# Kernel optimization log

Measured on AMD Instinct MI355X. Metric: run time of the kernel, lower is better.

Reference implementation:

```python
import jax, jax.numpy as jnp
import numpy as np

BIN_SIZE = 16
B, C, H, W = 32, 256, 64, 64


def _make_grid(lab):
    # Faithful vectorization of the per-batch loop in the torch module.
    # index = arange(bin) - bin//2
    idx = jnp.arange(BIN_SIZE, dtype=lab.dtype) - (BIN_SIZE // 2)
    # mesh_y[b, j] = 2*idx[j]*lab[b,0,3]/bin + (lab[b,0,1]*2 - 1)
    mesh_y = 2.0 * idx[None, :] * lab[:, 0, 3, None] / BIN_SIZE + (lab[:, 0, 1, None] * 2.0 - 1.0)
    # mesh_x[b, i] = 2*idx[i]*lab[b,0,4]/bin + (lab[b,0,2]*2 - 1)
    mesh_x = 2.0 * idx[None, :] * lab[:, 0, 4, None] / BIN_SIZE + (lab[:, 0, 2, None] * 2.0 - 1.0)
    b = lab.shape[0]
    # torch: grid_x, grid_y = meshgrid(mesh_x, mesh_y) with 'ij' indexing;
    # mesh_box[b,i,j,0] = grid_y[i,j] = mesh_y[j]; mesh_box[b,i,j,1] = grid_x[i,j] = mesh_x[i]
    g0 = jnp.broadcast_to(mesh_y[:, None, :], (b, BIN_SIZE, BIN_SIZE))  # x-coord channel
    g1 = jnp.broadcast_to(mesh_x[:, :, None], (b, BIN_SIZE, BIN_SIZE))  # y-coord channel
    return jnp.stack([g0, g1], axis=-1)  # [B, bin, bin, 2]


def _grid_sample(feat, grid):
    # Bilinear grid_sample, padding_mode='zeros', align_corners=False (torch defaults).
    Bb, Cc, Hh, Ww = feat.shape
    x = ((grid[..., 0] + 1.0) * Ww - 1.0) * 0.5  # [B, Hg, Wg]
    y = ((grid[..., 1] + 1.0) * Hh - 1.0) * 0.5
    x0f = jnp.floor(x)
    y0f = jnp.floor(y)
    x0 = x0f.astype(jnp.int32)
    y0 = y0f.astype(jnp.int32)
    x1 = x0 + 1
    y1 = y0 + 1
    wx1 = x - x0f
    wx0 = 1.0 - wx1
    wy1 = y - y0f
    wy0 = 1.0 - wy1
    bidx = jnp.arange(Bb)[:, None, None]

    def corner(xi, yi, wgt):
        valid = ((xi >= 0) & (xi < Ww) & (yi >= 0) & (yi < Hh)).astype(feat.dtype)
        xc = jnp.clip(xi, 0, Ww - 1)
        yc = jnp.clip(yi, 0, Hh - 1)
        v = feat[bidx, :, yc, xc]  # [B, Hg, Wg, C] (advanced indices pulled front)
        return v * (wgt * valid)[..., None]

    out = (corner(x0, y0, wx0 * wy0) + corner(x1, y0, wx1 * wy0)
           + corner(x0, y1, wx0 * wy1) + corner(x1, y1, wx1 * wy1))
    return jnp.transpose(out, (0, 3, 1, 2))  # [B, C, Hg, Wg]


def setup_inputs() -> dict:
    key = jax.random.key(0)
    k1, k2, k3 = jax.random.split(key, 3)
    original_features = jax.random.normal(k1, (B, C, H, W), dtype=jnp.float32)
    attack_features = jax.random.uniform(k2, (B, C, H, W), dtype=jnp.float32)
    lab = jax.random.uniform(k3, (B, 1, 5), dtype=jnp.float32)  # normalized box coords
    return {"original_features": original_features, "lab": lab, "attack_features": attack_features}


def reference(original_features, lab, attack_features):
    grid = _make_grid(lab)
    output_1 = _grid_sample(original_features, grid)
    output_2 = _grid_sample(attack_features, grid)
    return (output_1, output_2)
```

## Files before the change

kernel.cpp:

```cpp
#include <hip/hip_runtime.h>

#define Bsz 32
#define Csz 256
#define Hsz 64
#define Wsz 64
#define BIN 16

__global__ __launch_bounds__(256) void roi_feature_kernel(
    const float* __restrict__ orig,
    const float* __restrict__ lab,
    const float* __restrict__ attk,
    float* __restrict__ out)
{
    const int tid = blockIdx.x * blockDim.x + threadIdx.x;
    const int j = tid & (BIN - 1);
    const int i = (tid >> 4) & (BIN - 1);
    const int c = (tid >> 8) & (Csz - 1);
    const int b = tid >> 16;

    const float* lb = lab + b * 5;
    const float l1 = lb[1], l2 = lb[2], l3 = lb[3], l4 = lb[4];

    const float x = 2.0f * (float)(j - BIN / 2) * l3 / (float)BIN * (float)Wsz
                    + ((l1 * 2.0f - 1.0f + 1.0f) * (float)Wsz - 1.0f) * 0.5f
                    - (2.0f * (float)(j - BIN / 2) * l3 / (float)BIN) * (float)Wsz * 0.5f;
    const float gx = 2.0f * (float)(j - BIN / 2) * l3 / (float)BIN + (l1 * 2.0f - 1.0f);
    const float gy = 2.0f * (float)(i - BIN / 2) * l4 / (float)BIN + (l2 * 2.0f - 1.0f);
    const float xr = ((gx + 1.0f) * (float)Wsz - 1.0f) * 0.5f;
    const float yr = ((gy + 1.0f) * (float)Hsz - 1.0f) * 0.5f;
    (void)x;

    const float x0f = floorf(xr);
    const float y0f = floorf(yr);
    const int x0 = (int)x0f;
    const int y0 = (int)y0f;
    const int x1 = x0 + 1;
    const int y1 = y0 + 1;
    const float wx1 = xr - x0f, wx0 = 1.0f - wx1;
    const float wy1 = yr - y0f, wy0 = 1.0f - wy1;

    const size_t plane = (size_t)(b * Csz + c) * (Hsz * Wsz);
    const float* __restrict__ f0 = orig + plane;
    const float* __restrict__ f1 = attk + plane;

    float acc0 = 0.0f, acc1 = 0.0f;
#pragma unroll
    for (int k = 0; k < 4; ++k) {
        const int xi = (k & 1) ? x1 : x0;
        const int yi = (k & 2) ? y1 : y0;
        const float w = ((k & 1) ? wx1 : wx0) * ((k & 2) ? wy1 : wy0);
        const bool valid = (xi >= 0) && (xi < Wsz) && (yi >= 0) && (yi < Hsz);
        const int xc = min(max(xi, 0), Wsz - 1);
        const int yc = min(max(yi, 0), Hsz - 1);
        const float wv = valid ? w : 0.0f;
        const int off = yc * Wsz + xc;
        acc0 += f0[off] * wv;
        acc1 += f1[off] * wv;
    }

    __builtin_nontemporal_store(acc0, out + tid);
    __builtin_nontemporal_store(acc1, out + tid + (size_t)Bsz * Csz * BIN * BIN);
}

extern "C" void kernel_launch(void* const* d_in, const int* in_sizes, int n_in,
                              void* d_out, int out_size, void* d_ws, size_t ws_size,
                              hipStream_t stream) {
    const float* orig = (const float*)d_in[0];
    const float* lab  = (const float*)d_in[1];
    const float* attk = (const float*)d_in[2];
    float* out = (float*)d_out;

    const int total = Bsz * Csz * BIN * BIN;
    roi_feature_kernel<<<total / 256, 256, 0, stream>>>(orig, lab, attk, out);
}
```

Measured before the change: 236.5 us.

## Stage ROI window of feature planes into LDS with vectorized loads

Assigns one block per batch-channel plane, computes the bounding box of the sampling grid, and cooperatively copies that window of both feature maps into padded shared memory using float4 loads. Bilinear taps then read from LDS instead of issuing scattered global gathers. This trades gather inefficiency for extra LDS usage, a barrier, and possibly loading unused pixels inside the window.

```diff
diff --git a/kernel.cpp b/kernel.cpp
--- a/kernel.cpp
+++ b/kernel.cpp
@@ -5,6 +5,7 @@
 #define Hsz 64
 #define Wsz 64
 #define BIN 16
+#define LDS_STRIDE 68
 
 __global__ __launch_bounds__(256) void roi_feature_kernel(
     const float* __restrict__ orig,
@@ -12,23 +13,59 @@
     const float* __restrict__ attk,
     float* __restrict__ out)
 {
-    const int tid = blockIdx.x * blockDim.x + threadIdx.x;
-    const int j = tid & (BIN - 1);
-    const int i = (tid >> 4) & (BIN - 1);
-    const int c = (tid >> 8) & (Csz - 1);
-    const int b = tid >> 16;
+    __shared__ float lds0[Hsz * LDS_STRIDE];
+    __shared__ float lds1[Hsz * LDS_STRIDE];
+
+    const int bc = blockIdx.x;
+    const int b  = bc >> 8;
+    const int t  = threadIdx.x;
+    const int j  = t & (BIN - 1);
+    const int i  = t >> 4;
 
     const float* lb = lab + b * 5;
     const float l1 = lb[1], l2 = lb[2], l3 = lb[3], l4 = lb[4];
 
-    const float x = 2.0f * (float)(j - BIN / 2) * l3 / (float)BIN * (float)Wsz
-                    + ((l1 * 2.0f - 1.0f + 1.0f) * (float)Wsz - 1.0f) * 0.5f
-                    - (2.0f * (float)(j - BIN / 2) * l3 / (float)BIN) * (float)Wsz * 0.5f;
+    const float xr_a = ((2.0f * (float)(0  - BIN / 2) * l3 / (float)BIN + (l1 * 2.0f - 1.0f) + 1.0f) * (float)Wsz - 1.0f) * 0.5f;
+    const float xr_b = ((2.0f * (float)(15 - BIN / 2) * l3 / (float)BIN + (l1 * 2.0f - 1.0f) + 1.0f) * (float)Wsz - 1.0f) * 0.5f;
+    const float yr_a = ((2.0f * (float)(0  - BIN / 2) * l4 / (float)BIN + (l2 * 2.0f - 1.0f) + 1.0f) * (float)Hsz - 1.0f) * 0.5f;
+    const float yr_b = ((2.0f * (float)(15 - BIN / 2) * l4 / (float)BIN + (l2 * 2.0f - 1.0f) + 1.0f) * (float)Hsz - 1.0f) * 0.5f;
+
+    const int xlo = (int)floorf(fminf(xr_a, xr_b));
+    const int xhi = (int)floorf(fmaxf(xr_a, xr_b)) + 1;
+    const int ylo = (int)floorf(fminf(yr_a, yr_b));
+    const int yhi = (int)floorf(fmaxf(yr_a, yr_b)) + 1;
+
+    const int xs = min(max(xlo, 0), Wsz - 1);
+    const int xe = min(max(xhi, 0), Wsz - 1);
+    const int ys = min(max(ylo, 0), Hsz - 1);
+    const int ye = min(max(yhi, 0), Hsz - 1);
+
+    const int c0    = xs & ~3;
+    const int c1e   = xe | 3;
+    const int nf4   = ((c1e - c0) >> 2) + 1;
+    const int nrows = ye - ys + 1;
+
+    const size_t plane = (size_t)bc * (Hsz * Wsz);
+    const float* __restrict__ s0 = orig + plane + (ys * Wsz + c0);
+    const float* __restrict__ s1 = attk + plane + (ys * Wsz + c0);
+
+    const int slots = nrows << 4;
+    for (int k = t; k < slots; k += 256) {
+        const int r = k >> 4;
+        const int s = k & 15;
+        if (s < nf4) {
+            const float4 v0 = *(const float4*)(s0 + r * Wsz + s * 4);
+            const float4 v1 = *(const float4*)(s1 + r * Wsz + s * 4);
+            *(float4*)&lds0[r * LDS_STRIDE + s * 4] = v0;
+            *(float4*)&lds1[r * LDS_STRIDE + s * 4] = v1;
+        }
+    }
+    __syncthreads();
+
     const float gx = 2.0f * (float)(j - BIN / 2) * l3 / (float)BIN + (l1 * 2.0f - 1.0f);
     const float gy = 2.0f * (float)(i - BIN / 2) * l4 / (float)BIN + (l2 * 2.0f - 1.0f);
     const float xr = ((gx + 1.0f) * (float)Wsz - 1.0f) * 0.5f;
     const float yr = ((gy + 1.0f) * (float)Hsz - 1.0f) * 0.5f;
-    (void)x;
 
     const float x0f = floorf(xr);
     const float y0f = floorf(yr);
@@ -39,10 +76,6 @@
     const float wx1 = xr - x0f, wx0 = 1.0f - wx1;
     const float wy1 = yr - y0f, wy0 = 1.0f - wy1;
 
-    const size_t plane = (size_t)(b * Csz + c) * (Hsz * Wsz);
-    const float* __restrict__ f0 = orig + plane;
-    const float* __restrict__ f1 = attk + plane;
-
     float acc0 = 0.0f, acc1 = 0.0f;
 #pragma unroll
     for (int k = 0; k < 4; ++k) {
@@ -50,14 +83,15 @@
         const int yi = (k & 2) ? y1 : y0;
         const float w = ((k & 1) ? wx1 : wx0) * ((k & 2) ? wy1 : wy0);
         const bool valid = (xi >= 0) && (xi < Wsz) && (yi >= 0) && (yi < Hsz);
-        const int xc = min(max(xi, 0), Wsz - 1);
-        const int yc = min(max(yi, 0), Hsz - 1);
         const float wv = valid ? w : 0.0f;
-        const int off = yc * Wsz + xc;
-        acc0 += f0[off] * wv;
-        acc1 += f1[off] * wv;
+        const int lx = min(max(xi, c0), c1e) - c0;
+        const int ly = min(max(yi, ys), ye) - ys;
+        const int off = ly * LDS_STRIDE + lx;
+        acc0 += lds0[off] * wv;
+        acc1 += lds1[off] * wv;
     }
 
+    const int tid = bc * 256 + t;
     __builtin_nontemporal_store(acc0, out + tid);
     __builtin_nontemporal_store(acc1, out + tid + (size_t)Bsz * Csz * BIN * BIN);
 }
@@ -70,6 +104,6 @@
     const float* attk = (const float*)d_in[2];
     float* out = (float*)d_out;
 
-    const int total = Bsz * Csz * BIN * BIN;
-    roi_feature_kernel<<<total / 256, 256, 0, stream>>>(orig, lab, attk, out);
+    const int blocks = Bsz * Csz;
+    roi_feature_kernel<<<blocks, 256, 0, stream>>>(orig, lab, attk, out);
 }
```

Measured after the change: 239.3 us. Within noise of the previous version (+1.2%).
